# Kernel optimization log

Measured on AMD Instinct MI355X. Metric: run time of the kernel, lower is better.

The kernel has to match this reference:

```python
import jax, jax.numpy as jnp
import numpy as np

NEG_SLOPE = 0.2

def _gat_layer(x, src, dst, W, a_src, a_dst, b, n_nodes):
    # x: [N, Fin], W: [Fin, Fout], a_src/a_dst: [Fout], b: [Fout]
    h = x @ W                                  # [N, Fout]
    alpha_s = h @ a_src                        # [N]
    alpha_d = h @ a_dst                        # [N]
    e = jax.nn.leaky_relu(alpha_s[src] + alpha_d[dst], NEG_SLOPE)  # [E]
    # softmax over edges grouped by destination node
    m = jax.ops.segment_max(e, dst, num_segments=n_nodes)
    ex = jnp.exp(e - m[dst])
    denom = jax.ops.segment_sum(ex, dst, num_segments=n_nodes)
    alpha = ex / denom[dst]                    # [E]
    out = jax.ops.segment_sum(h[src] * alpha[:, None], dst, num_segments=n_nodes)
    return out + b


def setup_inputs() -> dict:
    key = jax.random.key(0)
    N, E, INP = 50000, 1600000, 128
    topo = [32, 64, 128, 128]
    OUT = 16
    ks = jax.random.split(key, 32)
    inp = {}
    inp['x'] = jax.random.normal(ks[0], (N, INP), dtype=jnp.float32)
    inp['edge_index'] = jax.random.randint(ks[1], (2, E), 0, N, dtype=jnp.int64)
    dims = [INP] + topo
    ki = 2
    for i in range(4):
        fin, fout = dims[i], dims[i + 1]
        s = 1.0 / np.sqrt(fin)
        inp[f'W{i}'] = jax.random.normal(ks[ki], (fin, fout), dtype=jnp.float32) * s; ki += 1
        inp[f'a_src{i}'] = jax.random.normal(ks[ki], (fout,), dtype=jnp.float32) * (1.0 / np.sqrt(fout)); ki += 1
        inp[f'a_dst{i}'] = jax.random.normal(ks[ki], (fout,), dtype=jnp.float32) * (1.0 / np.sqrt(fout)); ki += 1
        inp[f'b{i}'] = jnp.zeros((fout,), dtype=jnp.float32); ki += 1
    inp['fc_W'] = jax.random.normal(ks[ki], (topo[-1], OUT), dtype=jnp.float32) * (1.0 / np.sqrt(topo[-1])); ki += 1
    inp['fc_b'] = jnp.zeros((OUT,), dtype=jnp.float32)
    return inp


def reference(x, edge_index, W0, a_src0, a_dst0, b0, W1, a_src1, a_dst1, b1,
              W2, a_src2, a_dst2, b2, W3, a_src3, a_dst3, b3, fc_W, fc_b):
    n = x.shape[0]
    loops = jnp.arange(n, dtype=edge_index.dtype)
    src = jnp.concatenate([edge_index[0], loops])  # add self-loops (GATConv default)
    dst = jnp.concatenate([edge_index[1], loops])
    layers = [(W0, a_src0, a_dst0, b0), (W1, a_src1, a_dst1, b1),
              (W2, a_src2, a_dst2, b2), (W3, a_src3, a_dst3, b3)]
    for (W, a_s, a_d, b) in layers:
        x = jax.nn.relu(_gat_layer(x, src, dst, W, a_s, a_d, b, n))
    return x @ fc_W + fc_b
```

## Files before the change

kernel.cpp:

```cpp
#include <hip/hip_runtime.h>
#include <hip/hip_bf16.h>
#include <hip/hip_fp16.h>


__device__ __forceinline__ float bf2f(unsigned short w) {
    return __uint_as_float(((unsigned int)w) << 16);
}
__device__ __forceinline__ unsigned enc_f(float f) {
    unsigned u = __float_as_uint(f);
    return (u & 0x80000000u) ? ~u : (u | 0x80000000u);
}
__device__ __forceinline__ float dec_f(unsigned u) {
    unsigned v = (u & 0x80000000u) ? (u & 0x7FFFFFFFu) : ~u;
    return __uint_as_float(v);
}

#define ELL_K 96
#define NCHUNK 256

__global__ void detect_kernel(const unsigned short* __restrict__ xw,
                              const int* __restrict__ ew,
                              int* __restrict__ flags,
                              unsigned* __restrict__ maxbuf)
{
    __shared__ int cnt_sane[256];
    __shared__ int cnt_nz[256];
    const int t = threadIdx.x;
    unsigned short w = xw[2 * t];
    int e = (w >> 7) & 0xff;
    cnt_sane[t] = (e >= 110 && e <= 133) ? 1 : 0;
    cnt_nz[t] = (ew[2 * t + 1] != 0) ? 1 : 0;
    if (t < 8) maxbuf[t] = 0u;
    __syncthreads();
    if (t == 0) {
        int s = 0, nz = 0;
        for (int i = 0; i < 256; ++i) { s += cnt_sane[i]; nz += cnt_nz[i]; }
        flags[0] = (s >= 128) ? 1 : 0;
        flags[1] = (nz == 0) ? 1 : 0;
    }
}

struct ParamPtrs {
    const void* src[18];
    int n[18];
    int off[18];
};

__global__ void convert_params_kernel(ParamPtrs pp, const int* __restrict__ flags,
                                      float* __restrict__ out, float* __restrict__ wsd)
{
    const int b = blockIdx.x;
    const int bf = flags[0];
    if (b < 18) {
        const int n = pp.n[b];
        const float* fp = (const float*)pp.src[b];
        const unsigned short* hp = (const unsigned short*)pp.src[b];
        float* o = out + pp.off[b];
        for (int i = threadIdx.x; i < n; i += blockDim.x)
            o[i] = bf ? bf2f(hp[i]) : fp[i];
        return;
    }
    const int l = b - 18;
    const int wi = l ? 8 : 4;
    const unsigned short* Wh  = (const unsigned short*)pp.src[wi];
    const float*          Wf  = (const float*)pp.src[wi];
    const unsigned short* Ash = (const unsigned short*)pp.src[wi + 1];
    const float*          Asf = (const float*)pp.src[wi + 1];
    const unsigned short* Adh = (const unsigned short*)pp.src[wi + 2];
    const float*          Adf = (const float*)pp.src[wi + 2];
    const int FIN  = l ? 64 : 32;
    const int FOUT = l ? 128 : 64;
    float* ws = wsd + l * 256;
    float* wd = ws + 128;
    const int k = threadIdx.x;
    if (k < FIN) {
        float s = 0.f, d = 0.f;
        for (int j = 0; j < FOUT; ++j) {
            const float w = bf ? bf2f(Wh[k * FOUT + j]) : Wf[k * FOUT + j];
            const float a = bf ? bf2f(Ash[j]) : Asf[j];
            const float c = bf ? bf2f(Adh[j]) : Adf[j];
            s += w * a;
            d += w * c;
        }
        ws[k] = s;
        wd[k] = d;
    }
}

__global__ __launch_bounds__(256) void max_finalize_kernel(
    const float2* __restrict__ bm, int nb, unsigned* __restrict__ maxSD)
{
    __shared__ float sm[4][2];
    const int tx = threadIdx.x;
    float ms = -INFINITY, md = -INFINITY;
    for (int i = tx; i < nb; i += 256) {
        const float2 v = bm[i];
        ms = fmaxf(ms, v.x);
        md = fmaxf(md, v.y);
    }
    #pragma unroll
    for (int off = 32; off > 0; off >>= 1) {
        ms = fmaxf(ms, __shfl_down(ms, off, 64));
        md = fmaxf(md, __shfl_down(md, off, 64));
    }
    if ((tx & 63) == 0) { sm[tx >> 6][0] = ms; sm[tx >> 6][1] = md; }
    __syncthreads();
    if (tx == 0) {
        #pragma unroll
        for (int w = 1; w < 4; ++w) {
            ms = fmaxf(ms, sm[w][0]);
            md = fmaxf(md, sm[w][1]);
        }
        maxSD[0] = enc_f(ms);
        maxSD[1] = enc_f(md);
    }
}

__global__ __launch_bounds__(1024) void hist_pack_kernel(
    const int* __restrict__ e, const int* __restrict__ flags,
    unsigned* __restrict__ sd, unsigned* __restrict__ hist,
    long long E, long long Et, int chunk, int NQ)
{
    extern __shared__ unsigned hcnt[];
    const int c = blockIdx.x;
    for (int i = threadIdx.x; i < NQ; i += 1024) hcnt[i] = 0u;
    __syncthreads();
    const int f64 = flags[1];
    const long long c0 = (long long)c * chunk;
    long long c1 = c0 + chunk; if (c1 > Et) c1 = Et;
    for (long long t = c0 + threadIdx.x; t < c1; t += 1024) {
        int s, d;
        if (t >= E) { s = (int)(t - E); d = s; }
        else if (f64) { s = e[2 * t]; d = e[2 * E + 2 * t]; }
        else          { s = e[t];     d = e[E + t]; }
        sd[t] = (unsigned)s | ((unsigned)d << 16);
        atomicAdd(&hcnt[d >> 2], 1u << ((d & 3) << 3));
    }
    __syncthreads();
    unsigned* hrow = hist + (size_t)c * NQ;
    for (int i = threadIdx.x; i < NQ; i += 1024) hrow[i] = hcnt[i];
}

__global__ __launch_bounds__(256) void chunk_scan_kernel(
    const unsigned* __restrict__ hist, unsigned* __restrict__ base32,
    int* __restrict__ deg, int NQ, int N)
{
    __shared__ unsigned short sums[32][8][4];
    const int dql = threadIdx.x & 31;
    const int oct = threadIdx.x >> 5;
    const int dq  = blockIdx.x * 32 + dql;
    const int cbeg = oct * 32;

    unsigned s0 = 0, s1 = 0, s2 = 0, s3 = 0;
    if (dq < NQ) {
        const unsigned* hp = hist + (size_t)cbeg * NQ + dq;
        #pragma unroll 8
        for (int c = 0; c < 32; ++c) {
            const unsigned v = hp[(size_t)c * NQ];
            s0 += v & 0xffu;          s1 += (v >> 8) & 0xffu;
            s2 += (v >> 16) & 0xffu;  s3 += v >> 24;
        }
    }
    sums[dql][oct][0] = (unsigned short)s0;
    sums[dql][oct][1] = (unsigned short)s1;
    sums[dql][oct][2] = (unsigned short)s2;
    sums[dql][oct][3] = (unsigned short)s3;
    __syncthreads();

    unsigned r0 = 0, r1 = 0, r2 = 0, r3 = 0;
    #pragma unroll
    for (int p = 0; p < 8; ++p) {
        if (p < oct) {
            r0 += sums[dql][p][0]; r1 += sums[dql][p][1];
            r2 += sums[dql][p][2]; r3 += sums[dql][p][3];
        }
    }
    if (dq >= NQ) return;

    if (oct == 7) {
        const int d0 = dq * 4;
        const int t0 = (int)(r0 + s0), t1 = (int)(r1 + s1);
        const int t2 = (int)(r2 + s2), t3 = (int)(r3 + s3);
        if (d0 + 3 < N) {
            *(int4*)(deg + d0) = make_int4(t0, t1, t2, t3);
        } else {
            if (d0     < N) deg[d0]     = t0;
            if (d0 + 1 < N) deg[d0 + 1] = t1;
            if (d0 + 2 < N) deg[d0 + 2] = t2;
            if (d0 + 3 < N) deg[d0 + 3] = t3;
        }
    }

    unsigned run0 = r0, run1 = r1, run2 = r2, run3 = r3;
    const unsigned* hp = hist + (size_t)cbeg * NQ + dq;
    unsigned* bp = base32 + (size_t)cbeg * NQ + dq;
    for (int c = 0; c < 32; ++c) {
        const unsigned v = hp[(size_t)c * NQ];
        const unsigned o = (run0 < 255u ? run0 : 255u)
                         | ((run1 < 255u ? run1 : 255u) << 8)
                         | ((run2 < 255u ? run2 : 255u) << 16)
                         | ((run3 < 255u ? run3 : 255u) << 24);
        bp[(size_t)c * NQ] = o;
        run0 += v & 0xffu;          run1 += (v >> 8) & 0xffu;
        run2 += (v >> 16) & 0xffu;  run3 += v >> 24;
    }
}

__global__ __launch_bounds__(256) void ell_fill_kernel(
    const unsigned* __restrict__ sd, const unsigned* __restrict__ base32,
    unsigned short* __restrict__ ell16, long long Et, int chunk, int NQ, int shift)
{
    extern __shared__ unsigned cnt[];
    const int bucket = blockIdx.x & 7;
    const int c = blockIdx.x >> 3;
    const int words = (1 << shift) >> 2;
    for (int i = threadIdx.x; i < words; i += 256) cnt[i] = 0u;
    __syncthreads();
    const long long c0 = (long long)c * chunk;
    long long c1 = c0 + chunk; if (c1 > Et) c1 = Et;
    const unsigned* brow = base32 + (size_t)c * NQ;
    const int dlo = bucket << shift;
    for (long long i = c0 + threadIdx.x; i < c1; i += 256) {
        const unsigned v = sd[i];
        const int d = (int)(v >> 16);
        if ((d >> shift) != bucket) continue;
        const int dl = d - dlo;
        const unsigned sh = (unsigned)((dl & 3) << 3);
        const unsigned old = atomicAdd(&cnt[dl >> 2], 1u << sh);
        const unsigned lr = (old >> sh) & 0xffu;
        const unsigned b = (brow[d >> 2] >> ((d & 3) << 3)) & 0xffu;
        const unsigned slot = b + lr;
        if (slot < ELL_K)
            ell16[(long long)d * ELL_K + slot] = (unsigned short)(v & 0xffffu);
    }
}

struct Half4 { __half2 a, b; };

__device__ __forceinline__ void store4(float* h, long long idx, const float* a) {
    *(float4*)(h + idx) = make_float4(a[0], a[1], a[2], a[3]);
}
__device__ __forceinline__ void store4(__half* h, long long idx, const float* a) {
    Half4 v;
    v.a = __floats2half2_rn(a[0], a[1]);
    v.b = __floats2half2_rn(a[2], a[3]);
    *(Half4*)(h + idx) = v;
}

template <int FIN, int FOUT, typename OT>
__global__ __launch_bounds__(256) void gemm_alpha_kernel(
    const void* __restrict__ xv, const int* __restrict__ flags, int x_ext,
    const float* __restrict__ W, const float* __restrict__ a_src,
    const float* __restrict__ a_dst, const float* __restrict__ bias,
    OT* __restrict__ h,
    float* __restrict__ alpha_s, float* __restrict__ alpha_d,
    float2* __restrict__ blkmax, int has_alpha,
    int N, int relu_in, int has_bias, int relu_alpha)
{
    constexpr int CG = FOUT / 4;
    constexpr int RT = 256 / CG;
    constexpr int RR = 64 / RT;
    constexpr int TM = 64;
    constexpr int XP = FIN + 4;
    constexpr int Q  = FIN / 8;

    __shared__ float xs[TM * XP];
    __shared__ float red[2][TM][CG + 1];

    const int tx = threadIdx.x;
    const int cg = tx & (CG - 1);
    const int rt = tx / CG;
    const long long base = (long long)blockIdx.x * TM;

    const int xbf = x_ext ? flags[0] : 0;

    for (int idx = tx; idx < TM * Q; idx += 256) {
        const int r  = idx / Q;
        const int c8 = idx - r * Q;
        const long long grow = base + r;
        float v[8] = {0.f, 0.f, 0.f, 0.f, 0.f, 0.f, 0.f, 0.f};
        if (grow < N) {
            const long long gi = grow * FIN + 8 * c8;
            if (x_ext) {
                if (xbf) {
                    const unsigned short* xp = (const unsigned short*)xv + gi;
                    #pragma unroll
                    for (int u = 0; u < 8; ++u) v[u] = bf2f(xp[u]);
                } else {
                    const float4 f0 = *((const float4*)((const float*)xv + gi));
                    const float4 f1 = *((const float4*)((const float*)xv + gi + 4));
                    v[0] = f0.x; v[1] = f0.y; v[2] = f0.z; v[3] = f0.w;
                    v[4] = f1.x; v[5] = f1.y; v[6] = f1.z; v[7] = f1.w;
                }
            } else {
                const float4 raw = *((const float4*)((const __half*)xv + gi));
                const __half2* q = (const __half2*)&raw;
                const float2 a0 = __half22float2(q[0]);
                const float2 a1 = __half22float2(q[1]);
                const float2 a2 = __half22float2(q[2]);
                const float2 a3 = __half22float2(q[3]);
                v[0] = a0.x; v[1] = a0.y; v[2] = a1.x; v[3] = a1.y;
                v[4] = a2.x; v[5] = a2.y; v[6] = a3.x; v[7] = a3.y;
            }
            if (relu_in) {
                #pragma unroll
                for (int u = 0; u < 8; ++u) v[u] = fmaxf(v[u], 0.f);
            }
        }
        *(float4*)&xs[r * XP + 8 * c8]     = make_float4(v[0], v[1], v[2], v[3]);
        *(float4*)&xs[r * XP + 8 * c8 + 4] = make_float4(v[4], v[5], v[6], v[7]);
    }
    __syncthreads();

    float acc[RR][4];
    #pragma unroll
    for (int rr = 0; rr < RR; ++rr)
        { acc[rr][0] = acc[rr][1] = acc[rr][2] = acc[rr][3] = 0.f; }

    const int r0 = rt * RR;
    #pragma unroll 4
    for (int k = 0; k < FIN; ++k) {
        const float4 w4 = *(const float4*)(W + k * FOUT + 4 * cg);
        #pragma unroll
        for (int rr = 0; rr < RR; ++rr) {
            const float xval = xs[(r0 + rr) * XP + k];
            acc[rr][0] += xval * w4.x;
            acc[rr][1] += xval * w4.y;
            acc[rr][2] += xval * w4.z;
            acc[rr][3] += xval * w4.w;
        }
    }

    if (has_bias) {
        const float4 b4 = *(const float4*)(bias + 4 * cg);
        #pragma unroll
        for (int rr = 0; rr < RR; ++rr) {
            acc[rr][0] += b4.x; acc[rr][1] += b4.y;
            acc[rr][2] += b4.z; acc[rr][3] += b4.w;
        }
    }

    #pragma unroll
    for (int rr = 0; rr < RR; ++rr) {
        const long long grow = base + r0 + rr;
        if (grow < N)
            store4(h, grow * FOUT + 4 * cg, acc[rr]);
    }

    if (has_alpha) {
        const float4 as4 = *(const float4*)(a_src + 4 * cg);
        const float4 ad4 = *(const float4*)(a_dst + 4 * cg);
        #pragma unroll
        for (int rr = 0; rr < RR; ++rr) {
            float b0 = acc[rr][0], b1 = acc[rr][1], b2 = acc[rr][2], b3 = acc[rr][3];
            if (relu_alpha) {
                b0 = fmaxf(b0, 0.f); b1 = fmaxf(b1, 0.f);
                b2 = fmaxf(b2, 0.f); b3 = fmaxf(b3, 0.f);
            }
            red[0][r0 + rr][cg] = b0 * as4.x + b1 * as4.y + b2 * as4.z + b3 * as4.w;
            red[1][r0 + rr][cg] = b0 * ad4.x + b1 * ad4.y + b2 * ad4.z + b3 * ad4.w;
        }
        __syncthreads();
        if (tx < TM) {
            float ss = 0.f, sd = 0.f;
            #pragma unroll
            for (int j = 0; j < CG; ++j) {
                ss += red[0][tx][j];
                sd += red[1][tx][j];
            }
            const long long grow = base + tx;
            const bool valid = grow < N;
            if (valid) { alpha_s[grow] = ss; alpha_d[grow] = sd; }
            float ms = valid ? ss : -INFINITY;
            float md = valid ? sd : -INFINITY;
            #pragma unroll
            for (int off = 32; off > 0; off >>= 1) {
                ms = fmaxf(ms, __shfl_down(ms, off, 64));
                md = fmaxf(md, __shfl_down(md, off, 64));
            }
            if (tx == 0)
                blkmax[blockIdx.x] = make_float2(ms, md);
        }
    }
}

template <int F, int XRELU, int ADDB, int AFUSE>
__global__ __launch_bounds__(256) void gat_gather_kernel(
    const int* __restrict__ deg, const unsigned short* __restrict__ ell16,
    const float* __restrict__ as, const float* __restrict__ ad,
    const unsigned* __restrict__ maxSD,
    const __half* __restrict__ h, const float* __restrict__ bias,
    __half* __restrict__ out, int N,
    const float* __restrict__ wsA, const float* __restrict__ wdA,
    float* __restrict__ asO, float* __restrict__ adO,
    float2* __restrict__ bmax)
{
    constexpr int LPE = F / 8;
    constexpr int EPJ = 64 / LPE;

    const int wslot = threadIdx.x >> 6;
    const int lane = threadIdx.x & 63;
    const int d = blockIdx.x * 4 + wslot;
    const bool dvalid = d < N;
    if (!AFUSE && !dvalid) return;

    float ssA = -INFINITY, sdA = -INFINITY;

    if (dvalid) {
        const float M = dec_f(maxSD[0]) + dec_f(maxSD[1]);
        const int cnt_all = min(deg[d], ELL_K);
        const long long e0 = (long long)d * ELL_K;
        const float add = ad[d];

        const int sub = lane / LPE;
        const int fl  = (lane % LPE) * 8;

        float den = 0.f;
        float a0 = 0.f, a1 = 0.f, a2 = 0.f, a3 = 0.f;
        float a4 = 0.f, a5 = 0.f, a6 = 0.f, a7 = 0.f;
        for (int base = 0; base < cnt_all; base += 64) {
            const int e = base + lane;
            float p = 0.f;
            int s = 0;
            if (e < cnt_all) {
                s = (int)ell16[e0 + e];
                float v = as[s] + add;
                v = (v > 0.f) ? v : 0.2f * v;
                p = expf(v - M);
            }
            den += p;
            const int cnt = min(64, cnt_all - base);
            for (int j = 0; j < cnt; j += 4 * EPJ) {
                float pj[4];
                float4 hv[4];
                #pragma unroll
                for (int u = 0; u < 4; ++u) {
                    const int jj = j + u * EPJ + sub;
                    pj[u] = __shfl(p, jj, 64);
                    const int sj = __shfl(s, jj, 64);
                    hv[u] = *(const float4*)(h + (long long)sj * F + fl);
                }
                #pragma unroll
                for (int u = 0; u < 4; ++u) {
                    const __half2* q = (const __half2*)&hv[u];
                    float2 f0 = __half22float2(q[0]);
                    float2 f1 = __half22float2(q[1]);
                    float2 f2 = __half22float2(q[2]);
                    float2 f3 = __half22float2(q[3]);
                    if (XRELU) {
                        f0.x = fmaxf(f0.x, 0.f); f0.y = fmaxf(f0.y, 0.f);
                        f1.x = fmaxf(f1.x, 0.f); f1.y = fmaxf(f1.y, 0.f);
                        f2.x = fmaxf(f2.x, 0.f); f2.y = fmaxf(f2.y, 0.f);
                        f3.x = fmaxf(f3.x, 0.f); f3.y = fmaxf(f3.y, 0.f);
                    }
                    a0 += pj[u] * f0.x;  a1 += pj[u] * f0.y;
                    a2 += pj[u] * f1.x;  a3 += pj[u] * f1.y;
                    a4 += pj[u] * f2.x;  a5 += pj[u] * f2.y;
                    a6 += pj[u] * f3.x;  a7 += pj[u] * f3.y;
                }
            }
        }
        #pragma unroll
        for (int off = 32; off > 0; off >>= 1)
            den += __shfl_down(den, off, 64);
        den = __shfl(den, 0, 64);
        const float inv = 1.f / den;

        #pragma unroll
        for (int off = 32; off >= LPE; off >>= 1) {
            a0 += __shfl_down(a0, off, 64);
            a1 += __shfl_down(a1, off, 64);
            a2 += __shfl_down(a2, off, 64);
            a3 += __shfl_down(a3, off, 64);
            a4 += __shfl_down(a4, off, 64);
            a5 += __shfl_down(a5, off, 64);
            a6 += __shfl_down(a6, off, 64);
            a7 += __shfl_down(a7, off, 64);
        }
        if (lane < LPE) {
            float v0, v1, v2, v3, v4, v5, v6, v7;
            if (ADDB) {
                const float4 bA = *(const float4*)(bias + fl);
                const float4 bB = *(const float4*)(bias + fl + 4);
                v0 = bA.x + a0 * inv;  v1 = bA.y + a1 * inv;
                v2 = bA.z + a2 * inv;  v3 = bA.w + a3 * inv;
                v4 = bB.x + a4 * inv;  v5 = bB.y + a5 * inv;
                v6 = bB.z + a6 * inv;  v7 = bB.w + a7 * inv;
            } else {
                v0 = a0 * inv;  v1 = a1 * inv;  v2 = a2 * inv;  v3 = a3 * inv;
                v4 = a4 * inv;  v5 = a5 * inv;  v6 = a6 * inv;  v7 = a7 * inv;
            }
            float4 pack;
            __half2* q = (__half2*)&pack;
            q[0] = __floats2half2_rn(v0, v1);
            q[1] = __floats2half2_rn(v2, v3);
            q[2] = __floats2half2_rn(v4, v5);
            q[3] = __floats2half2_rn(v6, v7);
            *(float4*)(out + (long long)d * F + fl) = pack;

            if (AFUSE) {
                const float4 wA = *(const float4*)(wsA + fl);
                const float4 wB = *(const float4*)(wsA + fl + 4);
                const float4 dA = *(const float4*)(wdA + fl);
                const float4 dB = *(const float4*)(wdA + fl + 4);
                const float r0 = fmaxf(v0, 0.f), r1 = fmaxf(v1, 0.f);
                const float r2 = fmaxf(v2, 0.f), r3 = fmaxf(v3, 0.f);
                const float r4 = fmaxf(v4, 0.f), r5 = fmaxf(v5, 0.f);
                const float r6 = fmaxf(v6, 0.f), r7 = fmaxf(v7, 0.f);
                float ss = r0 * wA.x + r1 * wA.y + r2 * wA.z + r3 * wA.w
                         + r4 * wB.x + r5 * wB.y + r6 * wB.z + r7 * wB.w;
                float sd = r0 * dA.x + r1 * dA.y + r2 * dA.z + r3 * dA.w
                         + r4 * dB.x + r5 * dB.y + r6 * dB.z + r7 * dB.w;
                #pragma unroll
                for (int off = LPE / 2; off > 0; off >>= 1) {
                    ss += __shfl_down(ss, off, 64);
                    sd += __shfl_down(sd, off, 64);
                }
                if (lane == 0) {
                    asO[d] = ss;
                    adO[d] = sd;
                    ssA = ss;
                    sdA = sd;
                }
            }
        }
    }

    if (AFUSE) {
        __shared__ float smx[4][2];
        if (lane == 0) {
            smx[wslot][0] = dvalid ? ssA : -INFINITY;
            smx[wslot][1] = dvalid ? sdA : -INFINITY;
        }
        __syncthreads();
        if (threadIdx.x == 0) {
            float ms = smx[0][0], md = smx[0][1];
            #pragma unroll
            for (int w = 1; w < 4; ++w) {
                ms = fmaxf(ms, smx[w][0]);
                md = fmaxf(md, smx[w][1]);
            }
            bmax[blockIdx.x] = make_float2(ms, md);
        }
    }
}

extern "C" void kernel_launch(void* const* d_in, const int* in_sizes, int n_in,
                              void* d_out, int out_size, void* d_ws, size_t ws_size,
                              hipStream_t stream)
{
    const int INP = 128;
    const int N = in_sizes[0] / INP;
    const long long E = in_sizes[1] / 2;
    const long long Et = E + N;

    const int Fin[4]  = {128, 32, 64, 128};
    const int Fout[4] = {32, 64, 128, 128};

    const int NQ = (N + 3) / 4;
    const size_t histBytes = (size_t)NQ * 4 * NCHUNK;
    const size_t xbufBytes = (size_t)N * 128 * sizeof(__half);
    const size_t bigBytes  = histBytes > xbufBytes ? histBytes : xbufBytes;

    char* p = (char*)d_ws;
    auto alloc = [&](size_t bytes) {
        char* r = p;
        p += (bytes + 255) & ~(size_t)255;
        return r;
    };
    __half*   bufH    = (__half*)  alloc(bigBytes);
    __half*   bufX    = (__half*)  alloc(bigBytes);
    float*    as      = (float*)   alloc((size_t)N * sizeof(float));
    float*    ad      = (float*)   alloc((size_t)N * sizeof(float));
    float*    as2     = (float*)   alloc((size_t)N * sizeof(float));
    float*    ad2     = (float*)   alloc((size_t)N * sizeof(float));
    int*      deg     = (int*)     alloc((size_t)N * sizeof(int));
    unsigned short* ell16 = (unsigned short*)alloc((size_t)N * ELL_K * sizeof(unsigned short));
    unsigned* sd      = (unsigned*)alloc((size_t)Et * sizeof(unsigned));
    unsigned* maxbuf  = (unsigned*)alloc(64);
    int*      flags   = (int*)     alloc(64);
    float*    wsd     = (float*)   alloc(512 * sizeof(float));
    float2*   blkmax  = (float2*)  alloc(16384 * sizeof(float2));
    float*    params  = (float*)   alloc(64 * 1024 * sizeof(float));
    (void)ws_size;

    unsigned* hist   = (unsigned*)bufH;
    unsigned* base32 = (unsigned*)bufX;

    detect_kernel<<<1, 256, 0, stream>>>((const unsigned short*)d_in[0],
                                         (const int*)d_in[1], flags, maxbuf);

    ParamPtrs pp;
    int off = 0;
    {
        int k = 0;
        for (int i = 0; i < 4; ++i) {
            pp.n[k++] = Fin[i] * Fout[i];
            pp.n[k++] = Fout[i];
            pp.n[k++] = Fout[i];
            pp.n[k++] = Fout[i];
        }
        pp.n[16] = 128 * 16;
        pp.n[17] = 16;
        for (int i = 0; i < 18; ++i) {
            pp.src[i] = d_in[2 + i];
            pp.off[i] = off;
            off += pp.n[i];
        }
    }
    convert_params_kernel<<<20, 256, 0, stream>>>(pp, flags, params, wsd);

    const float* Wl[4], *asr[4], *adt[4], *bl[4];
    for (int i = 0; i < 4; ++i) {
        Wl[i]  = params + pp.off[4 * i + 0];
        asr[i] = params + pp.off[4 * i + 1];
        adt[i] = params + pp.off[4 * i + 2];
        bl[i]  = params + pp.off[4 * i + 3];
    }
    const float* fcW = params + pp.off[16];
    const float* fcb = params + pp.off[17];

    const int* e32 = (const int*)d_in[1];

    {
        const int chunk = (int)((Et + NCHUNK - 1) / NCHUNK);
        int shift = 0;
        while ((N >> shift) > 8) shift++;
        hist_pack_kernel<<<NCHUNK, 1024, (size_t)NQ * 4, stream>>>(
            e32, flags, sd, hist, E, Et, chunk, NQ);
        chunk_scan_kernel<<<(NQ + 31) / 32, 256, 0, stream>>>(
            hist, base32, deg, NQ, N);
        ell_fill_kernel<<<NCHUNK * 8, 256, (size_t)(1 << shift), stream>>>(
            sd, base32, ell16, Et, chunk, NQ, shift);
    }

    const int gblocks = (N + 3) / 4;
    const int mblocks = (N + 63) / 64;
    const void* xin = d_in[0];

    gemm_alpha_kernel<128, 32, __half><<<mblocks, 256, 0, stream>>>(
        xin, flags, 1, Wl[0], asr[0], adt[0], nullptr, bufH, as, ad,
        blkmax, 1, N, 0, 0, 0);
    max_finalize_kernel<<<1, 256, 0, stream>>>(blkmax, mblocks, maxbuf + 0);
    gat_gather_kernel<32, 0, 1, 1><<<gblocks, 256, 0, stream>>>(
        deg, ell16, as, ad, maxbuf + 0, bufH, bl[0], bufX, N,
        wsd + 0, wsd + 128, as2, ad2, blkmax);
    max_finalize_kernel<<<1, 256, 0, stream>>>(blkmax, gblocks, maxbuf + 2);

    gat_gather_kernel<32, 1, 0, 0><<<gblocks, 256, 0, stream>>>(
        deg, ell16, as2, ad2, maxbuf + 2, bufX, nullptr, bufH, N,
        nullptr, nullptr, nullptr, nullptr, nullptr);
    gemm_alpha_kernel<32, 64, __half><<<mblocks, 256, 0, stream>>>(
        bufH, flags, 0, Wl[1], wsd + 256, wsd + 384, bl[1], bufX, as, ad,
        blkmax, 1, N, 0, 1, 1);
    max_finalize_kernel<<<1, 256, 0, stream>>>(blkmax, mblocks, maxbuf + 4);

    gat_gather_kernel<64, 1, 0, 0><<<gblocks, 256, 0, stream>>>(
        deg, ell16, as, ad, maxbuf + 4, bufX, nullptr, bufH, N,
        nullptr, nullptr, nullptr, nullptr, nullptr);
    gemm_alpha_kernel<64, 128, __half><<<mblocks, 256, 0, stream>>>(
        bufH, flags, 0, Wl[2], nullptr, nullptr, bl[2], bufX, nullptr, nullptr,
        nullptr, 0, N, 0, 1, 0);

    gemm_alpha_kernel<128, 128, __half><<<mblocks, 256, 0, stream>>>(
        bufX, flags, 0, Wl[3], asr[3], adt[3], nullptr, bufH, as, ad,
        blkmax, 1, N, 1, 0, 0);
    max_finalize_kernel<<<1, 256, 0, stream>>>(blkmax, mblocks, maxbuf + 6);
    gat_gather_kernel<128, 0, 1, 0><<<gblocks, 256, 0, stream>>>(
        deg, ell16, as, ad, maxbuf + 6, bufH, bl[3], bufX, N,
        nullptr, nullptr, nullptr, nullptr, nullptr);

    gemm_alpha_kernel<128, 16, float><<<mblocks, 256, 0, stream>>>(
        bufX, flags, 0, fcW, nullptr, nullptr, fcb,
        (float*)d_out, nullptr, nullptr, nullptr, 0, N, 1, 1, 0);
}
```

Before: 456.2 us.

## Fuse per-node dense transforms into gather epilogues, removing three GEMM launches

```diff
diff --git a/kernel.cpp b/kernel.cpp
--- a/kernel.cpp
+++ b/kernel.cpp
@@ -384,7 +384,7 @@
     }
 }
 
-template <int F, int XRELU, int ADDB, int AFUSE>
+template <int F, int XRELU, int ADDB, int AFUSE, int GF>
 __global__ __launch_bounds__(256) void gat_gather_kernel(
     const int* __restrict__ deg, const unsigned short* __restrict__ ell16,
     const float* __restrict__ as, const float* __restrict__ ad,
@@ -393,18 +393,25 @@
     __half* __restrict__ out, int N,
     const float* __restrict__ wsA, const float* __restrict__ wdA,
     float* __restrict__ asO, float* __restrict__ adO,
-    float2* __restrict__ bmax)
+    float2* __restrict__ bmax,
+    const float* __restrict__ Wn, const float* __restrict__ bn,
+    float* __restrict__ outF)
 {
     constexpr int LPE = F / 8;
     constexpr int EPJ = 64 / LPE;
+    constexpr bool BMAX = (AFUSE != 0) || (GF == 64);
 
     const int wslot = threadIdx.x >> 6;
     const int lane = threadIdx.x & 63;
     const int d = blockIdx.x * 4 + wslot;
     const bool dvalid = d < N;
-    if (!AFUSE && !dvalid) return;
+    if (!BMAX && !dvalid) return;
 
     float ssA = -INFINITY, sdA = -INFINITY;
+
+    float inv = 0.f;
+    float a0 = 0.f, a1 = 0.f, a2 = 0.f, a3 = 0.f;
+    float a4 = 0.f, a5 = 0.f, a6 = 0.f, a7 = 0.f;
 
     if (dvalid) {
         const float M = dec_f(maxSD[0]) + dec_f(maxSD[1]);
@@ -416,8 +423,6 @@
         const int fl  = (lane % LPE) * 8;
 
         float den = 0.f;
-        float a0 = 0.f, a1 = 0.f, a2 = 0.f, a3 = 0.f;
-        float a4 = 0.f, a5 = 0.f, a6 = 0.f, a7 = 0.f;
         for (int base = 0; base < cnt_all; base += 64) {
             const int e = base + lane;
             float p = 0.f;
@@ -464,7 +469,7 @@
         for (int off = 32; off > 0; off >>= 1)
             den += __shfl_down(den, off, 64);
         den = __shfl(den, 0, 64);
-        const float inv = 1.f / den;
+        inv = 1.f / den;
 
         #pragma unroll
         for (int off = 32; off >= LPE; off >>= 1) {
@@ -477,56 +482,164 @@
             a6 += __shfl_down(a6, off, 64);
             a7 += __shfl_down(a7, off, 64);
         }
-        if (lane < LPE) {
-            float v0, v1, v2, v3, v4, v5, v6, v7;
-            if (ADDB) {
-                const float4 bA = *(const float4*)(bias + fl);
-                const float4 bB = *(const float4*)(bias + fl + 4);
-                v0 = bA.x + a0 * inv;  v1 = bA.y + a1 * inv;
-                v2 = bA.z + a2 * inv;  v3 = bA.w + a3 * inv;
-                v4 = bB.x + a4 * inv;  v5 = bB.y + a5 * inv;
-                v6 = bB.z + a6 * inv;  v7 = bB.w + a7 * inv;
-            } else {
-                v0 = a0 * inv;  v1 = a1 * inv;  v2 = a2 * inv;  v3 = a3 * inv;
-                v4 = a4 * inv;  v5 = a5 * inv;  v6 = a6 * inv;  v7 = a7 * inv;
-            }
-            float4 pack;
-            __half2* q = (__half2*)&pack;
-            q[0] = __floats2half2_rn(v0, v1);
-            q[1] = __floats2half2_rn(v2, v3);
-            q[2] = __floats2half2_rn(v4, v5);
-            q[3] = __floats2half2_rn(v6, v7);
-            *(float4*)(out + (long long)d * F + fl) = pack;
-
-            if (AFUSE) {
-                const float4 wA = *(const float4*)(wsA + fl);
-                const float4 wB = *(const float4*)(wsA + fl + 4);
-                const float4 dA = *(const float4*)(wdA + fl);
-                const float4 dB = *(const float4*)(wdA + fl + 4);
-                const float r0 = fmaxf(v0, 0.f), r1 = fmaxf(v1, 0.f);
-                const float r2 = fmaxf(v2, 0.f), r3 = fmaxf(v3, 0.f);
-                const float r4 = fmaxf(v4, 0.f), r5 = fmaxf(v5, 0.f);
-                const float r6 = fmaxf(v6, 0.f), r7 = fmaxf(v7, 0.f);
-                float ss = r0 * wA.x + r1 * wA.y + r2 * wA.z + r3 * wA.w
-                         + r4 * wB.x + r5 * wB.y + r6 * wB.z + r7 * wB.w;
-                float sd = r0 * dA.x + r1 * dA.y + r2 * dA.z + r3 * dA.w
-                         + r4 * dB.x + r5 * dB.y + r6 * dB.z + r7 * dB.w;
+
+        if (GF == 0) {
+            if (lane < LPE) {
+                const int fl2 = fl;
+                float v0, v1, v2, v3, v4, v5, v6, v7;
+                if (ADDB) {
+                    const float4 bA = *(const float4*)(bias + fl2);
+                    const float4 bB = *(const float4*)(bias + fl2 + 4);
+                    v0 = bA.x + a0 * inv;  v1 = bA.y + a1 * inv;
+                    v2 = bA.z + a2 * inv;  v3 = bA.w + a3 * inv;
+                    v4 = bB.x + a4 * inv;  v5 = bB.y + a5 * inv;
+                    v6 = bB.z + a6 * inv;  v7 = bB.w + a7 * inv;
+                } else {
+                    v0 = a0 * inv;  v1 = a1 * inv;  v2 = a2 * inv;  v3 = a3 * inv;
+                    v4 = a4 * inv;  v5 = a5 * inv;  v6 = a6 * inv;  v7 = a7 * inv;
+                }
+                float4 pack;
+                __half2* q = (__half2*)&pack;
+                q[0] = __floats2half2_rn(v0, v1);
+                q[1] = __floats2half2_rn(v2, v3);
+                q[2] = __floats2half2_rn(v4, v5);
+                q[3] = __floats2half2_rn(v6, v7);
+                *(float4*)(out + (long long)d * F + fl2) = pack;
+
+                if (AFUSE) {
+                    const float4 wA = *(const float4*)(wsA + fl2);
+                    const float4 wB = *(const float4*)(wsA + fl2 + 4);
+                    const float4 dA = *(const float4*)(wdA + fl2);
+                    const float4 dB = *(const float4*)(wdA + fl2 + 4);
+                    const float r0 = fmaxf(v0, 0.f), r1 = fmaxf(v1, 0.f);
+                    const float r2 = fmaxf(v2, 0.f), r3 = fmaxf(v3, 0.f);
+                    const float r4 = fmaxf(v4, 0.f), r5 = fmaxf(v5, 0.f);
+                    const float r6 = fmaxf(v6, 0.f), r7 = fmaxf(v7, 0.f);
+                    float ss = r0 * wA.x + r1 * wA.y + r2 * wA.z + r3 * wA.w
+                             + r4 * wB.x + r5 * wB.y + r6 * wB.z + r7 * wB.w;
+                    float sdv = r0 * dA.x + r1 * dA.y + r2 * dA.z + r3 * dA.w
+                              + r4 * dB.x + r5 * dB.y + r6 * dB.z + r7 * dB.w;
+                    #pragma unroll
+                    for (int off = LPE / 2; off > 0; off >>= 1) {
+                        ss  += __shfl_down(ss, off, 64);
+                        sdv += __shfl_down(sdv, off, 64);
+                    }
+                    if (lane == 0) {
+                        asO[d] = ss;
+                        adO[d] = sdv;
+                        ssA = ss;
+                        sdA = sdv;
+                    }
+                }
+            }
+        } else if (GF == 64) {
+            float xo = bn[lane];
+            #define GSTEP(L, R) { const float y = __shfl(a##R, L, 64) * inv; \
+                                  xo += y * Wn[((L) * 8 + (R)) * 64 + lane]; }
+            GSTEP(0,0) GSTEP(0,1) GSTEP(0,2) GSTEP(0,3)
+            GSTEP(0,4) GSTEP(0,5) GSTEP(0,6) GSTEP(0,7)
+            GSTEP(1,0) GSTEP(1,1) GSTEP(1,2) GSTEP(1,3)
+            GSTEP(1,4) GSTEP(1,5) GSTEP(1,6) GSTEP(1,7)
+            GSTEP(2,0) GSTEP(2,1) GSTEP(2,2) GSTEP(2,3)
+            GSTEP(2,4) GSTEP(2,5) GSTEP(2,6) GSTEP(2,7)
+            GSTEP(3,0) GSTEP(3,1) GSTEP(3,2) GSTEP(3,3)
+            GSTEP(3,4) GSTEP(3,5) GSTEP(3,6) GSTEP(3,7)
+            #undef GSTEP
+            out[(long long)d * 64 + lane] = __float2half(xo);
+            const float r = fmaxf(xo, 0.f);
+            float ss = r * wsA[lane];
+            float sdv = r * wdA[lane];
+            #pragma unroll
+            for (int off = 32; off > 0; off >>= 1) {
+                ss  += __shfl_down(ss, off, 64);
+                sdv += __shfl_down(sdv, off, 64);
+            }
+            if (lane == 0) {
+                asO[d] = ss;
+                adO[d] = sdv;
+                ssA = ss;
+                sdA = sdv;
+            }
+        } else if (GF == 128) {
+            float xo0 = bn[2 * lane], xo1 = bn[2 * lane + 1];
+            #define GSTEP(L, R) { const float y = __shfl(a##R, L, 64) * inv; \
+                                  const float2 wv = *(const float2*)(Wn + ((L) * 8 + (R)) * 128 + 2 * lane); \
+                                  xo0 += y * wv.x; xo1 += y * wv.y; }
+            GSTEP(0,0) GSTEP(0,1) GSTEP(0,2) GSTEP(0,3)
+            GSTEP(0,4) GSTEP(0,5) GSTEP(0,6) GSTEP(0,7)
+            GSTEP(1,0) GSTEP(1,1) GSTEP(1,2) GSTEP(1,3)
+            GSTEP(1,4) GSTEP(1,5) GSTEP(1,6) GSTEP(1,7)
+            GSTEP(2,0) GSTEP(2,1) GSTEP(2,2) GSTEP(2,3)
+            GSTEP(2,4) GSTEP(2,5) GSTEP(2,6) GSTEP(2,7)
+            GSTEP(3,0) GSTEP(3,1) GSTEP(3,2) GSTEP(3,3)
+            GSTEP(3,4) GSTEP(3,5) GSTEP(3,6) GSTEP(3,7)
+            GSTEP(4,0) GSTEP(4,1) GSTEP(4,2) GSTEP(4,3)
+            GSTEP(4,4) GSTEP(4,5) GSTEP(4,6) GSTEP(4,7)
+            GSTEP(5,0) GSTEP(5,1) GSTEP(5,2) GSTEP(5,3)
+            GSTEP(5,4) GSTEP(5,5) GSTEP(5,6) GSTEP(5,7)
+            GSTEP(6,0) GSTEP(6,1) GSTEP(6,2) GSTEP(6,3)
+            GSTEP(6,4) GSTEP(6,5) GSTEP(6,6) GSTEP(6,7)
+            GSTEP(7,0) GSTEP(7,1) GSTEP(7,2) GSTEP(7,3)
+            GSTEP(7,4) GSTEP(7,5) GSTEP(7,6) GSTEP(7,7)
+            #undef GSTEP
+            *(__half2*)(out + (long long)d * 128 + 2 * lane) =
+                __floats2half2_rn(xo0, xo1);
+        } else {
+            float pacc[8];
+            float r[8];
+            bool have = false;
+            if (lane < LPE) {
+                const int fl2 = fl;
+                const float4 bA = *(const float4*)(bias + fl2);
+                const float4 bB = *(const float4*)(bias + fl2 + 4);
+                r[0] = fmaxf(bA.x + a0 * inv, 0.f);
+                r[1] = fmaxf(bA.y + a1 * inv, 0.f);
+                r[2] = fmaxf(bA.z + a2 * inv, 0.f);
+                r[3] = fmaxf(bA.w + a3 * inv, 0.f);
+                r[4] = fmaxf(bB.x + a4 * inv, 0.f);
+                r[5] = fmaxf(bB.y + a5 * inv, 0.f);
+                r[6] = fmaxf(bB.z + a6 * inv, 0.f);
+                r[7] = fmaxf(bB.w + a7 * inv, 0.f);
+                have = true;
+            }
+            #pragma unroll
+            for (int hi = 0; hi < 2; ++hi) {
                 #pragma unroll
-                for (int off = LPE / 2; off > 0; off >>= 1) {
-                    ss += __shfl_down(ss, off, 64);
-                    sd += __shfl_down(sd, off, 64);
+                for (int j = 0; j < 8; ++j) pacc[j] = 0.f;
+                if (have) {
+                    #pragma unroll
+                    for (int k = 0; k < 8; ++k) {
+                        const float4 wA = *(const float4*)(Wn + (fl + k) * 16 + hi * 8);
+                        const float4 wB = *(const float4*)(Wn + (fl + k) * 16 + hi * 8 + 4);
+                        pacc[0] += r[k] * wA.x;  pacc[1] += r[k] * wA.y;
+                        pacc[2] += r[k] * wA.z;  pacc[3] += r[k] * wA.w;
+                        pacc[4] += r[k] * wB.x;  pacc[5] += r[k] * wB.y;
+                        pacc[6] += r[k] * wB.z;  pacc[7] += r[k] * wB.w;
+                    }
+                }
+                #pragma unroll
+                for (int off = 8; off > 0; off >>= 1) {
+                    #pragma unroll
+                    for (int j = 0; j < 8; ++j)
+                        pacc[j] += __shfl_down(pacc[j], off, 64);
                 }
                 if (lane == 0) {
-                    asO[d] = ss;
-                    adO[d] = sd;
-                    ssA = ss;
-                    sdA = sd;
+                    float4 o0 = make_float4(pacc[0] + bn[hi * 8 + 0],
+                                            pacc[1] + bn[hi * 8 + 1],
+                                            pacc[2] + bn[hi * 8 + 2],
+                                            pacc[3] + bn[hi * 8 + 3]);
+                    float4 o1 = make_float4(pacc[4] + bn[hi * 8 + 4],
+                                            pacc[5] + bn[hi * 8 + 5],
+                                            pacc[6] + bn[hi * 8 + 6],
+                                            pacc[7] + bn[hi * 8 + 7]);
+                    *(float4*)(outF + (long long)d * 16 + hi * 8)     = o0;
+                    *(float4*)(outF + (long long)d * 16 + hi * 8 + 4) = o1;
                 }
             }
         }
     }
 
-    if (AFUSE) {
+    if (BMAX) {
         __shared__ float smx[4][2];
         if (lane == 0) {
             smx[wslot][0] = dvalid ? ssA : -INFINITY;
@@ -642,35 +755,25 @@
         xin, flags, 1, Wl[0], asr[0], adt[0], nullptr, bufH, as, ad,
         blkmax, 1, N, 0, 0, 0);
     max_finalize_kernel<<<1, 256, 0, stream>>>(blkmax, mblocks, maxbuf + 0);
-    gat_gather_kernel<32, 0, 1, 1><<<gblocks, 256, 0, stream>>>(
+    gat_gather_kernel<32, 0, 1, 1, 0><<<gblocks, 256, 0, stream>>>(
         deg, ell16, as, ad, maxbuf + 0, bufH, bl[0], bufX, N,
-        wsd + 0, wsd + 128, as2, ad2, blkmax);
+        wsd + 0, wsd + 128, as2, ad2, blkmax, nullptr, nullptr, nullptr);
     max_finalize_kernel<<<1, 256, 0, stream>>>(blkmax, gblocks, maxbuf + 2);
 
-    gat_gather_kernel<32, 1, 0, 0><<<gblocks, 256, 0, stream>>>(
+    gat_gather_kernel<32, 1, 0, 0, 64><<<gblocks, 256, 0, stream>>>(
         deg, ell16, as2, ad2, maxbuf + 2, bufX, nullptr, bufH, N,
-        nullptr, nullptr, nullptr, nullptr, nullptr);
-    gemm_alpha_kernel<32, 64, __half><<<mblocks, 256, 0, stream>>>(
-        bufH, flags, 0, Wl[1], wsd + 256, wsd + 384, bl[1], bufX, as, ad,
-        blkmax, 1, N, 0, 1, 1);
-    max_finalize_kernel<<<1, 256, 0, stream>>>(blkmax, mblocks, maxbuf + 4);
-
-    gat_gather_kernel<64, 1, 0, 0><<<gblocks, 256, 0, stream>>>(
-        deg, ell16, as, ad, maxbuf + 4, bufX, nullptr, bufH, N,
-        nullptr, nullptr, nullptr, nullptr, nullptr);
-    gemm_alpha_kernel<64, 128, __half><<<mblocks, 256, 0, stream>>>(
-        bufH, flags, 0, Wl[2], nullptr, nullptr, bl[2], bufX, nullptr, nullptr,
-        nullptr, 0, N, 0, 1, 0);
+        wsd + 256, wsd + 384, as, ad, blkmax, Wl[1], bl[1], nullptr);
+    max_finalize_kernel<<<1, 256, 0, stream>>>(blkmax, gblocks, maxbuf + 4);
+
+    gat_gather_kernel<64, 1, 0, 0, 128><<<gblocks, 256, 0, stream>>>(
+        deg, ell16, as, ad, maxbuf + 4, bufH, nullptr, bufX, N,
+        nullptr, nullptr, nullptr, nullptr, nullptr, Wl[2], bl[2], nullptr);
 
     gemm_alpha_kernel<128, 128, __half><<<mblocks, 256, 0, stream>>>(
         bufX, flags, 0, Wl[3], asr[3], adt[3], nullptr, bufH, as, ad,
         blkmax, 1, N, 1, 0, 0);
     max_finalize_kernel<<<1, 256, 0, stream>>>(blkmax, mblocks, maxbuf + 6);
-    gat_gather_kernel<128, 0, 1, 0><<<gblocks, 256, 0, stream>>>(
-        deg, ell16, as, ad, maxbuf + 6, bufH, bl[3], bufX, N,
-        nullptr, nullptr, nullptr, nullptr, nullptr);
-
-    gemm_alpha_kernel<128, 16, float><<<mblocks, 256, 0, stream>>>(
-        bufX, flags, 0, fcW, nullptr, nullptr, fcb,
-        (float*)d_out, nullptr, nullptr, nullptr, 0, N, 1, 1, 0);
-}
+    gat_gather_kernel<128, 0, 1, 0, 1><<<gblocks, 256, 0, stream>>>(
+        deg, ell16, as, ad, maxbuf + 6, bufH, bl[3], nullptr, N,
+        nullptr, nullptr, nullptr, nullptr, nullptr, fcW, fcb, (float*)d_out);
+}
```

After: 568.3 us. +24.6%, slower.
